# Performance work log

Measured on AMD Instinct MI355X. Metric: run time of the kernel, lower is better.

Reference implementation:

```python
import jax, jax.numpy as jnp
import numpy as np

N = 50000   # nodes
E = 800000  # edges
D = 64      # dim_node
H = 64      # hidden_channels
G = 512     # graphs in batch


def setup_inputs() -> dict:
    key = jax.random.key(0)
    ks = jax.random.split(key, 13)
    s = 0.05
    return dict(
        x=jax.random.normal(ks[0], (N, D), jnp.float32),
        edge_index=jax.random.randint(ks[1], (2, E), 0, N, dtype=jnp.int32),
        batch_idx=jnp.sort(jax.random.randint(ks[2], (N,), 0, G, dtype=jnp.int32)),
        W0=jax.random.normal(ks[3], (D, H), jnp.float32) * s,
        b0=jnp.zeros((H,), jnp.float32),
        W1=jax.random.normal(ks[4], (H, H), jnp.float32) * s,
        b1=jnp.zeros((H,), jnp.float32),
        W2=jax.random.normal(ks[5], (H, H), jnp.float32) * s,
        b2=jnp.zeros((H,), jnp.float32),
        lin1_w=jax.random.normal(ks[6], (H, H), jnp.float32) * s,
        lin1_b=jnp.zeros((H,), jnp.float32),
        lin2_w=jax.random.normal(ks[7], (H, 1), jnp.float32) * s,
        lin2_b=jnp.zeros((1,), jnp.float32),
    )


def gcn_conv(x, W, b, src, dst, n):
    """PyG GCNConv: out = D^{-1/2} (A + I) D^{-1/2} X W + b (self-loops added)."""
    h = x @ W                                   # [n, H] transform first (cheaper)
    loop = jnp.arange(n, dtype=src.dtype)
    row = jnp.concatenate([src, loop])          # message sources (incl. self-loops)
    col = jnp.concatenate([dst, loop])          # aggregation targets
    deg = jax.ops.segment_sum(jnp.ones_like(col, jnp.float32), col, num_segments=n)
    dinv = jnp.where(deg > 0, jax.lax.rsqrt(deg), 0.0)
    norm = dinv[row] * dinv[col]                # [E+n]
    msg = h[row] * norm[:, None]                # gather + scale
    return jax.ops.segment_sum(msg, col, num_segments=n) + b


def reference(x, edge_index, batch_idx, W0, b0, W1, b1, W2, b2,
              lin1_w, lin1_b, lin2_w, lin2_b):
    src, dst = edge_index[0], edge_index[1]
    h = jax.nn.relu(gcn_conv(x, W0, b0, src, dst, N))   # dropout(p=0, eval) = identity
    h = jax.nn.relu(gcn_conv(h, W1, b1, src, dst, N))
    h = jax.nn.relu(gcn_conv(h, W2, b2, src, dst, N))
    # global_mean_pool over graph ids
    sums = jax.ops.segment_sum(h, batch_idx, num_segments=G)            # [G, H]
    cnt = jax.ops.segment_sum(jnp.ones((N,), jnp.float32), batch_idx, num_segments=G)
    pooled = sums / jnp.maximum(cnt, 1.0)[:, None]
    h = jax.nn.relu(pooled @ lin1_w + lin1_b)
    return h @ lin2_w + lin2_b                                          # [G, 1]
```

## Files before the change

kernel.cpp:

```cpp
#include <hip/hip_runtime.h>
#include <math.h>

#define NN 50000
#define EE 800000
#define HH 64
#define GG 512
#define SCAN_NB ((NN + 1023) / 1024)


__global__ void k_deg(const int* __restrict__ dst, int* __restrict__ deg) {
    int e = blockIdx.x * blockDim.x + threadIdx.x;
    if (e < EE) atomicAdd(&deg[dst[e]], 1);
}


__global__ void __launch_bounds__(1024) k_scan1(const int* __restrict__ deg,
                                                int* __restrict__ rowptr,
                                                int* __restrict__ bsum,
                                                float* __restrict__ dinv) {
    int tid = threadIdx.x;
    int lane = tid & 63, w = tid >> 6;
    int i = blockIdx.x * 1024 + tid;
    int v = (i < NN) ? deg[i] : 0;
    if (i < NN) dinv[i] = 1.0f / sqrtf((float)(v + 1));
    int x = v;
#pragma unroll
    for (int off = 1; off < 64; off <<= 1) {
        int y = __shfl_up(x, off);
        if (lane >= off) x += y;
    }
    __shared__ int ws[16];
    if (lane == 63) ws[w] = x;
    __syncthreads();
    if (tid < 16) {
        int y = ws[tid];
        int z = y;
#pragma unroll
        for (int off = 1; off < 16; off <<= 1) {
            int t2 = __shfl_up(z, off);
            if (tid >= off) z += t2;
        }
        ws[tid] = z - y;
    }
    __syncthreads();
    int excl = x - v + ws[w];
    if (i < NN) rowptr[i] = excl;
    if (tid == 1023) bsum[blockIdx.x] = excl + v;
}

__global__ void __launch_bounds__(64) k_scan2(int* __restrict__ bsum) {
    int lane = threadIdx.x;
    int v = (lane < SCAN_NB) ? bsum[lane] : 0;
    int x = v;
#pragma unroll
    for (int off = 1; off < 64; off <<= 1) {
        int y = __shfl_up(x, off);
        if (lane >= off) x += y;
    }
    if (lane < SCAN_NB) bsum[lane] = x - v;
}

__global__ void __launch_bounds__(1024) k_scan3(int* __restrict__ rowptr,
                                                const int* __restrict__ bsum) {
    int i = blockIdx.x * 1024 + threadIdx.x;
    if (i < NN) rowptr[i] += bsum[blockIdx.x];
    if (i == 0) rowptr[NN] = EE;
}


__global__ void k_fill(const int* __restrict__ src, const int* __restrict__ dst,
                       const int* __restrict__ rowptr,
                       int* __restrict__ cursor, int* __restrict__ csr_src) {
    int e = blockIdx.x * blockDim.x + threadIdx.x;
    if (e >= EE) return;
    int d = dst[e];
    int pos = atomicAdd(&cursor[d], 1);
    csr_src[rowptr[d] + pos] = src[e];
}


template<bool RELU>
__global__ void __launch_bounds__(256) k_xform(const float* __restrict__ x,
                                               const float* __restrict__ W,
                                               const float* __restrict__ dinv,
                                               float* __restrict__ t) {
    __shared__ float sW[64 * 64];
    __shared__ float sX[32 * 65];
    int tid = threadIdx.x;
    for (int k = tid; k < 64 * 64; k += 256) sW[k] = W[k];
    int row0 = blockIdx.x * 32;
    for (int v = tid; v < 32 * 16; v += 256) {
        int r  = v >> 4;
        int k4 = (v & 15) * 4;
        int row = row0 + r;
        float4 val = make_float4(0.f, 0.f, 0.f, 0.f);
        if (row < NN) val = *(const float4*)(x + (size_t)row * 64 + k4);
        if (RELU) {
            val.x = fmaxf(val.x, 0.f); val.y = fmaxf(val.y, 0.f);
            val.z = fmaxf(val.z, 0.f); val.w = fmaxf(val.w, 0.f);
        }
        sX[r * 65 + k4 + 0] = val.x;
        sX[r * 65 + k4 + 1] = val.y;
        sX[r * 65 + k4 + 2] = val.z;
        sX[r * 65 + k4 + 3] = val.w;
    }
    __syncthreads();
    int r  = tid >> 3;
    int c0 = (tid & 7) * 8;
    float acc[8] = {0.f, 0.f, 0.f, 0.f, 0.f, 0.f, 0.f, 0.f};
    for (int k = 0; k < 64; ++k) {
        float xv = sX[r * 65 + k];
#pragma unroll
        for (int j = 0; j < 8; ++j) acc[j] = fmaf(xv, sW[k * 64 + c0 + j], acc[j]);
    }
    int row = row0 + r;
    if (row < NN) {
        float dv = dinv[row];
#pragma unroll
        for (int j = 0; j < 8; ++j) acc[j] *= dv;
        float4* o = (float4*)(t + (size_t)row * 64 + c0);
        o[0] = make_float4(acc[0], acc[1], acc[2], acc[3]);
        o[1] = make_float4(acc[4], acc[5], acc[6], acc[7]);
    }
}


template<bool POOL>
__global__ void __launch_bounds__(256) k_gather(const float* __restrict__ t,
                                                const float* __restrict__ dinv,
                                                const int* __restrict__ rowptr,
                                                const int* __restrict__ csr_src,
                                                const float* __restrict__ b,
                                                const int* __restrict__ batch,
                                                float* __restrict__ out) {
    int i = (blockIdx.x * blockDim.x + threadIdx.x) >> 6;
    int c = threadIdx.x & 63;
    if (i >= NN) return;
    float acc = t[(size_t)i * 64 + c];
    float a0 = 0.f, a1 = 0.f, a2 = 0.f, a3 = 0.f;
    int e = rowptr[i], end = rowptr[i + 1];
    for (; e + 8 <= end; e += 8) {
        int s0 = csr_src[e + 0], s1 = csr_src[e + 1];
        int s2 = csr_src[e + 2], s3 = csr_src[e + 3];
        int s4 = csr_src[e + 4], s5 = csr_src[e + 5];
        int s6 = csr_src[e + 6], s7 = csr_src[e + 7];
        float v0 = t[(size_t)s0 * 64 + c], v1 = t[(size_t)s1 * 64 + c];
        float v2 = t[(size_t)s2 * 64 + c], v3 = t[(size_t)s3 * 64 + c];
        float v4 = t[(size_t)s4 * 64 + c], v5 = t[(size_t)s5 * 64 + c];
        float v6 = t[(size_t)s6 * 64 + c], v7 = t[(size_t)s7 * 64 + c];
        a0 += v0 + v4; a1 += v1 + v5; a2 += v2 + v6; a3 += v3 + v7;
    }
    if (e + 4 <= end) {
        int s0 = csr_src[e + 0], s1 = csr_src[e + 1];
        int s2 = csr_src[e + 2], s3 = csr_src[e + 3];
        a0 += t[(size_t)s0 * 64 + c]; a1 += t[(size_t)s1 * 64 + c];
        a2 += t[(size_t)s2 * 64 + c]; a3 += t[(size_t)s3 * 64 + c];
        e += 4;
    }
    for (; e < end; ++e) a0 += t[(size_t)csr_src[e] * 64 + c];
    acc += (a0 + a1) + (a2 + a3);
    float r = fmaf(acc, dinv[i], b[c]);
    if (POOL) {
        atomicAdd(&out[(size_t)batch[i] * 64 + c], fmaxf(r, 0.0f));
    } else {
        out[(size_t)i * 64 + c] = r;
    }
}

__global__ void k_cnt(const int* __restrict__ batch, int* __restrict__ cnt) {
    int i = blockIdx.x * blockDim.x + threadIdx.x;
    if (i < NN) atomicAdd(&cnt[batch[i]], 1);
}


__global__ void __launch_bounds__(64) k_head(const float* __restrict__ pooled,
                                             const int* __restrict__ cnt,
                                             const float* __restrict__ w1,
                                             const float* __restrict__ b1,
                                             const float* __restrict__ w2,
                                             const float* __restrict__ b2,
                                             float* __restrict__ out) {
    int g = blockIdx.x;
    int c = threadIdx.x;
    __shared__ float sp[64];
    float cf = fmaxf((float)cnt[g], 1.0f);
    sp[c] = pooled[(size_t)g * 64 + c] / cf;
    __syncthreads();
    float acc = b1[c];
    for (int k = 0; k < 64; ++k) acc = fmaf(sp[k], w1[k * 64 + c], acc);
    float h1 = fmaxf(acc, 0.0f);
    float p = h1 * w2[c];
#pragma unroll
    for (int off = 32; off > 0; off >>= 1) p += __shfl_down(p, off);
    if (c == 0) out[g] = p + b2[0];
}


extern "C" void kernel_launch(void* const* d_in, const int* in_sizes, int n_in,
                              void* d_out, int out_size, void* d_ws, size_t ws_size,
                              hipStream_t stream) {
    const float* x      = (const float*)d_in[0];
    const int*   ei     = (const int*)d_in[1];
    const int*   batch  = (const int*)d_in[2];
    const float* W0     = (const float*)d_in[3];
    const float* b0     = (const float*)d_in[4];
    const float* W1     = (const float*)d_in[5];
    const float* b1     = (const float*)d_in[6];
    const float* W2     = (const float*)d_in[7];
    const float* b2     = (const float*)d_in[8];
    const float* lin1w  = (const float*)d_in[9];
    const float* lin1b  = (const float*)d_in[10];
    const float* lin2w  = (const float*)d_in[11];
    const float* lin2b  = (const float*)d_in[12];
    float* out = (float*)d_out;

    const int* src = ei;
    const int* dst = ei + EE;

    char* ws = (char*)d_ws;
    size_t off = 0;
    auto carve = [&](size_t bytes) {
        void* p = ws + off;
        off = (off + bytes + 255) & ~(size_t)255;
        return p;
    };
    int*   deg      = (int*)carve((size_t)NN * 4);
    int*   cursor   = (int*)carve((size_t)NN * 4);
    float* pooled   = (float*)carve((size_t)GG * 64 * 4);
    int*   cnt      = (int*)carve((size_t)GG * 4);
    size_t zero_span = off;
    float* dinv     = (float*)carve((size_t)NN * 4);
    int*   rowptr   = (int*)carve((size_t)(NN + 1) * 4);
    int*   bsum     = (int*)carve((size_t)SCAN_NB * 4);
    int*   csr_src  = (int*)carve((size_t)EE * 4);
    float* bufT     = (float*)carve((size_t)NN * 64 * 4);
    float* bufA     = (float*)carve((size_t)NN * 64 * 4);

    hipMemsetAsync(deg, 0, zero_span, stream);

    k_deg  <<<(EE + 255) / 256, 256, 0, stream>>>(dst, deg);
    k_scan1<<<SCAN_NB, 1024, 0, stream>>>(deg, rowptr, bsum, dinv);
    k_scan2<<<1, 64, 0, stream>>>(bsum);
    k_scan3<<<SCAN_NB, 1024, 0, stream>>>(rowptr, bsum);
    k_fill <<<(EE + 255) / 256, 256, 0, stream>>>(src, dst, rowptr, cursor, csr_src);
    k_cnt  <<<(NN + 255) / 256, 256, 0, stream>>>(batch, cnt);

    const int xgrid = (NN + 31) / 32;
    const int ggrid = (NN * 64 + 255) / 256;

    k_xform<false><<<xgrid, 256, 0, stream>>>(x, W0, dinv, bufT);
    k_gather<false><<<ggrid, 256, 0, stream>>>(bufT, dinv, rowptr, csr_src,
                                               b0, batch, bufA);
    k_xform<true><<<xgrid, 256, 0, stream>>>(bufA, W1, dinv, bufT);
    k_gather<false><<<ggrid, 256, 0, stream>>>(bufT, dinv, rowptr, csr_src,
                                               b1, batch, bufA);
    k_xform<true><<<xgrid, 256, 0, stream>>>(bufA, W2, dinv, bufT);
    k_gather<true><<<ggrid, 256, 0, stream>>>(bufT, dinv, rowptr, csr_src,
                                              b2, batch, pooled);

    k_head<<<GG, 64, 0, stream>>>(pooled, cnt, lin1w, lin1b, lin2w, lin2b, out);
}
```

Baseline: 356.5 us.

## Pad CSR rows to multiples of eight and fold scan fixup into consumers

Each node's CSR row is padded to a multiple of 8 entries. The padding points at a dummy node NN whose transformed features are zero, because dinv[NN] is 0. This lets the gather loop drop its 4-wide and scalar tails and use wave-uniform (readfirstlane) bounds. The separate scan-fixup kernel is removed: consumers add the block offset bsum themselves. The node-count kernel is merged into the fill kernel, so fewer launches are needed. The cost is extra padded edges, which all read the same zero row, and slightly larger buffers.

Result: faster. 341.5 us (-4.2%).

```diff
diff --git a/kernel.cpp b/kernel.cpp
--- a/kernel.cpp
+++ b/kernel.cpp
@@ -6,6 +6,7 @@
 #define HH 64
 #define GG 512
 #define SCAN_NB ((NN + 1023) / 1024)
+#define PE (EE + 7 * NN)
 
 
 __global__ void k_deg(const int* __restrict__ dst, int* __restrict__ deg) {
@@ -21,8 +22,10 @@
     int tid = threadIdx.x;
     int lane = tid & 63, w = tid >> 6;
     int i = blockIdx.x * 1024 + tid;
-    int v = (i < NN) ? deg[i] : 0;
-    if (i < NN) dinv[i] = 1.0f / sqrtf((float)(v + 1));
+    int d = (i < NN) ? deg[i] : 0;
+    if (i < NN)       dinv[i] = 1.0f / sqrtf((float)(d + 1));
+    else if (i == NN) dinv[i] = 0.0f;
+    int v = (i < NN) ? ((d + 7) & ~7) : 0;
     int x = v;
 #pragma unroll
     for (int off = 1; off < 64; off <<= 1) {
@@ -44,7 +47,7 @@
     }
     __syncthreads();
     int excl = x - v + ws[w];
-    if (i < NN) rowptr[i] = excl;
+    if (i <= NN) rowptr[i] = excl;
     if (tid == 1023) bsum[blockIdx.x] = excl + v;
 }
 
@@ -60,22 +63,26 @@
     if (lane < SCAN_NB) bsum[lane] = x - v;
 }
 
-__global__ void __launch_bounds__(1024) k_scan3(int* __restrict__ rowptr,
-                                                const int* __restrict__ bsum) {
-    int i = blockIdx.x * 1024 + threadIdx.x;
-    if (i < NN) rowptr[i] += bsum[blockIdx.x];
-    if (i == 0) rowptr[NN] = EE;
-}
-
 
 __global__ void k_fill(const int* __restrict__ src, const int* __restrict__ dst,
-                       const int* __restrict__ rowptr,
-                       int* __restrict__ cursor, int* __restrict__ csr_src) {
-    int e = blockIdx.x * blockDim.x + threadIdx.x;
-    if (e >= EE) return;
-    int d = dst[e];
-    int pos = atomicAdd(&cursor[d], 1);
-    csr_src[rowptr[d] + pos] = src[e];
+                       const int* __restrict__ rowptr, const int* __restrict__ bsum,
+                       const int* __restrict__ deg, const int* __restrict__ batch,
+                       int* __restrict__ cursor, int* __restrict__ csr_src,
+                       int* __restrict__ cnt) {
+    int tid = blockIdx.x * blockDim.x + threadIdx.x;
+    if (tid < EE) {
+        int d = dst[tid];
+        int pos = atomicAdd(&cursor[d], 1);
+        csr_src[rowptr[d] + bsum[d >> 10] + pos] = src[tid];
+    } else if (tid < EE + NN) {
+        int i = tid - EE;
+        int dg = deg[i];
+        int start = rowptr[i] + bsum[i >> 10] + dg;
+        int pad = ((dg + 7) & ~7) - dg;
+        for (int j = 0; j < pad; ++j) csr_src[start + j] = NN;
+    } else if (tid < EE + 2 * NN) {
+        atomicAdd(&cnt[batch[tid - EE - NN]], 1);
+    }
 }
 
 
@@ -114,7 +121,7 @@
         for (int j = 0; j < 8; ++j) acc[j] = fmaf(xv, sW[k * 64 + c0 + j], acc[j]);
     }
     int row = row0 + r;
-    if (row < NN) {
+    if (row <= NN) {
         float dv = dinv[row];
 #pragma unroll
         for (int j = 0; j < 8; ++j) acc[j] *= dv;
@@ -129,17 +136,19 @@
 __global__ void __launch_bounds__(256) k_gather(const float* __restrict__ t,
                                                 const float* __restrict__ dinv,
                                                 const int* __restrict__ rowptr,
+                                                const int* __restrict__ bsum,
                                                 const int* __restrict__ csr_src,
                                                 const float* __restrict__ b,
                                                 const int* __restrict__ batch,
                                                 float* __restrict__ out) {
-    int i = (blockIdx.x * blockDim.x + threadIdx.x) >> 6;
+    int i = __builtin_amdgcn_readfirstlane((blockIdx.x * blockDim.x + threadIdx.x) >> 6);
     int c = threadIdx.x & 63;
     if (i >= NN) return;
+    int e   = __builtin_amdgcn_readfirstlane(rowptr[i]     + bsum[i >> 10]);
+    int end = __builtin_amdgcn_readfirstlane(rowptr[i + 1] + bsum[(i + 1) >> 10]);
     float acc = t[(size_t)i * 64 + c];
     float a0 = 0.f, a1 = 0.f, a2 = 0.f, a3 = 0.f;
-    int e = rowptr[i], end = rowptr[i + 1];
-    for (; e + 8 <= end; e += 8) {
+    for (; e < end; e += 8) {
         int s0 = csr_src[e + 0], s1 = csr_src[e + 1];
         int s2 = csr_src[e + 2], s3 = csr_src[e + 3];
         int s4 = csr_src[e + 4], s5 = csr_src[e + 5];
@@ -150,14 +159,6 @@
         float v6 = t[(size_t)s6 * 64 + c], v7 = t[(size_t)s7 * 64 + c];
         a0 += v0 + v4; a1 += v1 + v5; a2 += v2 + v6; a3 += v3 + v7;
     }
-    if (e + 4 <= end) {
-        int s0 = csr_src[e + 0], s1 = csr_src[e + 1];
-        int s2 = csr_src[e + 2], s3 = csr_src[e + 3];
-        a0 += t[(size_t)s0 * 64 + c]; a1 += t[(size_t)s1 * 64 + c];
-        a2 += t[(size_t)s2 * 64 + c]; a3 += t[(size_t)s3 * 64 + c];
-        e += 4;
-    }
-    for (; e < end; ++e) a0 += t[(size_t)csr_src[e] * 64 + c];
     acc += (a0 + a1) + (a2 + a3);
     float r = fmaf(acc, dinv[i], b[c]);
     if (POOL) {
@@ -165,11 +166,6 @@
     } else {
         out[(size_t)i * 64 + c] = r;
     }
-}
-
-__global__ void k_cnt(const int* __restrict__ batch, int* __restrict__ cnt) {
-    int i = blockIdx.x * blockDim.x + threadIdx.x;
-    if (i < NN) atomicAdd(&cnt[batch[i]], 1);
 }
 
 
@@ -229,11 +225,11 @@
     float* pooled   = (float*)carve((size_t)GG * 64 * 4);
     int*   cnt      = (int*)carve((size_t)GG * 4);
     size_t zero_span = off;
-    float* dinv     = (float*)carve((size_t)NN * 4);
+    float* dinv     = (float*)carve((size_t)(NN + 1) * 4);
     int*   rowptr   = (int*)carve((size_t)(NN + 1) * 4);
     int*   bsum     = (int*)carve((size_t)SCAN_NB * 4);
-    int*   csr_src  = (int*)carve((size_t)EE * 4);
-    float* bufT     = (float*)carve((size_t)NN * 64 * 4);
+    int*   csr_src  = (int*)carve((size_t)PE * 4);
+    float* bufT     = (float*)carve((size_t)(NN + 1) * 64 * 4);
     float* bufA     = (float*)carve((size_t)NN * 64 * 4);
 
     hipMemsetAsync(deg, 0, zero_span, stream);
@@ -241,21 +237,21 @@
     k_deg  <<<(EE + 255) / 256, 256, 0, stream>>>(dst, deg);
     k_scan1<<<SCAN_NB, 1024, 0, stream>>>(deg, rowptr, bsum, dinv);
     k_scan2<<<1, 64, 0, stream>>>(bsum);
-    k_scan3<<<SCAN_NB, 1024, 0, stream>>>(rowptr, bsum);
-    k_fill <<<(EE + 255) / 256, 256, 0, stream>>>(src, dst, rowptr, cursor, csr_src);
-    k_cnt  <<<(NN + 255) / 256, 256, 0, stream>>>(batch, cnt);
-
-    const int xgrid = (NN + 31) / 32;
-    const int ggrid = (NN * 64 + 255) / 256;
+    k_fill <<<(EE + 2 * NN + 255) / 256, 256, 0, stream>>>(src, dst, rowptr, bsum,
+                                                           deg, batch, cursor,
+                                                           csr_src, cnt);
+
+    const int xgrid = (NN + 1 + 31) / 32;
+    const int ggrid = (NN * 64) / 256;
 
     k_xform<false><<<xgrid, 256, 0, stream>>>(x, W0, dinv, bufT);
-    k_gather<false><<<ggrid, 256, 0, stream>>>(bufT, dinv, rowptr, csr_src,
+    k_gather<false><<<ggrid, 256, 0, stream>>>(bufT, dinv, rowptr, bsum, csr_src,
                                                b0, batch, bufA);
     k_xform<true><<<xgrid, 256, 0, stream>>>(bufA, W1, dinv, bufT);
-    k_gather<false><<<ggrid, 256, 0, stream>>>(bufT, dinv, rowptr, csr_src,
+    k_gather<false><<<ggrid, 256, 0, stream>>>(bufT, dinv, rowptr, bsum, csr_src,
                                                b1, batch, bufA);
     k_xform<true><<<xgrid, 256, 0, stream>>>(bufA, W2, dinv, bufT);
-    k_gather<true><<<ggrid, 256, 0, stream>>>(bufT, dinv, rowptr, csr_src,
+    k_gather<true><<<ggrid, 256, 0, stream>>>(bufT, dinv, rowptr, bsum, csr_src,
                                               b2, batch, pooled);
 
     k_head<<<GG, 64, 0, stream>>>(pooled, cnt, lin1w, lin1b, lin2w, lin2b, out);
```
